# Performance work log

Hardware: AMD Instinct MI355X
Metric: run time of the kernel (lower is better)

Reference implementation:

```python
import jax, jax.numpy as jnp
import numpy as np

IN_DIM = 128
OUT_DIM = 128
B, N = 8, 2048
NEG_SLOPE = 0.2


def setup_inputs() -> dict:
    key = jax.random.key(0)
    k_h, k_adj, k_W, k_a = jax.random.split(key, 4)
    h = jax.random.normal(k_h, (B, N, IN_DIM), dtype=jnp.float32)
    adj = jax.random.randint(k_adj, (B, N, N), 0, 2, dtype=jnp.int32)
    # nn.Linear(in, out, bias=False): weight [out, in]
    W = jax.random.normal(k_W, (OUT_DIM, IN_DIM), dtype=jnp.float32) * (1.0 / np.sqrt(IN_DIM))
    # nn.Linear(2*out, 1, bias=False): weight [1, 2*out] -> store as vector [2*out]
    a = jax.random.normal(k_a, (2 * OUT_DIM,), dtype=jnp.float32) * (1.0 / np.sqrt(2 * OUT_DIM))
    return {"h": h, "adj": adj, "W": W, "a": a}


def reference(h, adj, W, a):
    # Wh: [B, N, Fo]
    Wh = jnp.einsum("bnf,of->bno", h, W)
    Fo = Wh.shape[-1]
    a_src, a_dst = a[:Fo], a[Fo:]
    # attn(cat([Wh_i, Wh_j])) == (Wh_i . a_src) + (Wh_j . a_dst) -- avoids [B,N,N,2F]
    s = Wh @ a_src  # [B, N]
    t = Wh @ a_dst  # [B, N]
    e = jax.nn.leaky_relu(s[:, :, None] + t[:, None, :], negative_slope=NEG_SLOPE)  # [B,N,N]
    e = jnp.where(adj == 0, -jnp.inf, e)
    alpha = jax.nn.softmax(e, axis=-1)
    alpha = jnp.nan_to_num(alpha, nan=0.0)  # rows with no neighbors -> 0
    return jnp.einsum("bnm,bmo->bno", alpha, Wh)
```

## Files before the change

kernel.cpp:

```cpp
#include <hip/hip_runtime.h>
#include <hip/hip_bf16.h>
#include <hip/hip_fp16.h>
#include <math.h>

#define B_ 8
#define N_ 2048
#define F_ 128

typedef __attribute__((ext_vector_type(8))) _Float16 half8;
typedef __attribute__((ext_vector_type(4))) float f32x4;

__global__ __launch_bounds__(256) void k_wh(
    const float* __restrict__ h, const float* __restrict__ W,
    const float* __restrict__ a,
    _Float16* __restrict__ WhH, float* __restrict__ sv, float* __restrict__ tv)
{
    __shared__ float h_s[64][129];
    __shared__ float Wt[128][68];
    __shared__ float wsm[128], wtm[128];
    __shared__ float sred[64][4], tred[64][4];

    const int t = threadIdx.x;
    const int rowblk = blockIdx.x >> 1;
    const int ohalf  = blockIdx.x & 1;
    const int r0 = rowblk * 64;

    {
        const int f = (t & 31) * 4;
        #pragma unroll
        for (int it = 0; it < 8; ++it) {
            const int r = (t >> 5) + it * 8;
            float4 v = *(const float4*)&h[(size_t)(r0 + r) * F_ + f];
            h_s[r][f] = v.x; h_s[r][f + 1] = v.y;
            h_s[r][f + 2] = v.z; h_s[r][f + 3] = v.w;
        }
    }
    {
        const int f = (t & 31) * 4;
        #pragma unroll
        for (int it = 0; it < 8; ++it) {
            const int o = (t >> 5) + it * 8;
            float4 v = *(const float4*)&W[(size_t)(ohalf * 64 + o) * F_ + f];
            Wt[f][o] = v.x; Wt[f + 1][o] = v.y;
            Wt[f + 2][o] = v.z; Wt[f + 3][o] = v.w;
        }
    }
    {
        const int f = t & 127;
        const int which = t >> 7;
        const float* av = a + which * 128;
        float acc = 0.f;
        for (int o = 0; o < 128; ++o)
            acc += W[(size_t)o * F_ + f] * av[o];
        if (which == 0) wsm[f] = acc; else wtm[f] = acc;
    }
    __syncthreads();

    const int o4 = t & 15;
    const int r4 = t >> 4;
    float acc[4][4];
    #pragma unroll
    for (int i = 0; i < 4; ++i)
        #pragma unroll
        for (int j = 0; j < 4; ++j) acc[i][j] = 0.f;

    #pragma unroll 4
    for (int k = 0; k < 128; ++k) {
        float4 w = *(const float4*)&Wt[k][o4 * 4];
        float h0 = h_s[r4 * 4 + 0][k];
        float h1 = h_s[r4 * 4 + 1][k];
        float h2 = h_s[r4 * 4 + 2][k];
        float h3 = h_s[r4 * 4 + 3][k];
        acc[0][0] += h0 * w.x; acc[0][1] += h0 * w.y; acc[0][2] += h0 * w.z; acc[0][3] += h0 * w.w;
        acc[1][0] += h1 * w.x; acc[1][1] += h1 * w.y; acc[1][2] += h1 * w.z; acc[1][3] += h1 * w.w;
        acc[2][0] += h2 * w.x; acc[2][1] += h2 * w.y; acc[2][2] += h2 * w.z; acc[2][3] += h2 * w.w;
        acc[3][0] += h3 * w.x; acc[3][1] += h3 * w.y; acc[3][2] += h3 * w.z; acc[3][3] += h3 * w.w;
    }

    {
        const int Rbase = r0 + r4 * 4;
        const int b    = Rbase >> 11;
        const int jj   = Rbase & 2047;
        const int jblk = jj >> 5;
        const int k8   = (jj >> 3) & 3;
        const int kk   = jj & 7;
        #pragma unroll
        for (int jo = 0; jo < 4; ++jo) {
            const int o = ohalf * 64 + o4 * 4 + jo;
            size_t off = ((size_t)(b * 64 + jblk) * 128 + o) * 32 + k8 * 8 + kk;
            union { _Float16 x[4]; uint2 u; } pk;
            pk.x[0] = (_Float16)acc[0][jo];
            pk.x[1] = (_Float16)acc[1][jo];
            pk.x[2] = (_Float16)acc[2][jo];
            pk.x[3] = (_Float16)acc[3][jo];
            *(uint2*)(WhH + off) = pk.u;
        }
    }

    {
        const int r = t & 63, part = t >> 6;
        float as_ = 0.f, at_ = 0.f;
        const int kb = part * 32;
        for (int k = kb; k < kb + 32; ++k) {
            float hv = h_s[r][k];
            as_ += hv * wsm[k];
            at_ += hv * wtm[k];
        }
        sred[r][part] = as_; tred[r][part] = at_;
    }
    __syncthreads();
    if (ohalf == 0 && t < 64) {
        sv[r0 + t] = sred[t][0] + sred[t][1] + sred[t][2] + sred[t][3];
        tv[r0 + t] = tred[t][0] + tred[t][1] + tred[t][2] + tred[t][3];
    }
}

__global__ __launch_bounds__(256, 4) void k_attn(
    const _Float16* __restrict__ WhH, const float* __restrict__ sv,
    const float* __restrict__ tv, const int* __restrict__ adj,
    float* __restrict__ out)
{
    __shared__ float redO[4][16][128];
    __shared__ float redL[4][16];
    __shared__ float tmr[4];

    const int t  = threadIdx.x;
    const int b  = blockIdx.x >> 7;
    const int i0 = (blockIdx.x & 127) * 16;
    const float* tb = tv + ((size_t)b << 11);

    float tm = -INFINITY;
    #pragma unroll
    for (int k = 0; k < 8; ++k) tm = fmaxf(tm, tb[t + k * 256]);
    #pragma unroll
    for (int k = 32; k; k >>= 1) tm = fmaxf(tm, __shfl_xor(tm, k, 64));
    if ((t & 63) == 0) tmr[t >> 6] = tm;
    __syncthreads();
    const float tmax = fmaxf(fmaxf(tmr[0], tmr[1]), fmaxf(tmr[2], tmr[3]));

    const int wv   = t >> 6;
    const int lane = t & 63;
    const int m_   = lane & 15;
    const int q_   = lane >> 4;

    const float s_i = sv[((size_t)b << 11) + i0 + m_];
    const float M_i = fmaxf(s_i + tmax, 0.f);

    const int jbase = wv * 512;
    const int* arow = adj + ((size_t)(((b << 11) + i0 + m_)) << 11) + q_ * 8;
    const float* tq = tb + q_ * 8;
    const _Float16* wbase = WhH + (((size_t)b * 64) << 12)
                          + (size_t)m_ * 32 + q_ * 8;

    f32x4 acc[8];
    #pragma unroll
    for (int n = 0; n < 8; ++n) acc[n] = (f32x4){0.f, 0.f, 0.f, 0.f};
    float lsum = 0.f;

    int4 aL = *(const int4*)&arow[jbase];
    int4 aH = *(const int4*)&arow[jbase + 4];

    for (int jj = 0; jj < 16; ++jj) {
        const int j0 = jbase + jj * 32;
        const int jn = jbase + ((jj + 1) & 15) * 32;
        int4 naL = *(const int4*)&arow[jn];
        int4 naH = *(const int4*)&arow[jn + 4];

        float4 tL = *(const float4*)&tq[j0];
        float4 tH = *(const float4*)&tq[j0 + 4];

        float e, p[8];
        e = s_i + tL.x; e = fmaxf(e, 0.2f * e); p[0] = aL.x ? __expf(e - M_i) : 0.f;
        e = s_i + tL.y; e = fmaxf(e, 0.2f * e); p[1] = aL.y ? __expf(e - M_i) : 0.f;
        e = s_i + tL.z; e = fmaxf(e, 0.2f * e); p[2] = aL.z ? __expf(e - M_i) : 0.f;
        e = s_i + tL.w; e = fmaxf(e, 0.2f * e); p[3] = aL.w ? __expf(e - M_i) : 0.f;
        e = s_i + tH.x; e = fmaxf(e, 0.2f * e); p[4] = aH.x ? __expf(e - M_i) : 0.f;
        e = s_i + tH.y; e = fmaxf(e, 0.2f * e); p[5] = aH.y ? __expf(e - M_i) : 0.f;
        e = s_i + tH.z; e = fmaxf(e, 0.2f * e); p[6] = aH.z ? __expf(e - M_i) : 0.f;
        e = s_i + tH.w; e = fmaxf(e, 0.2f * e); p[7] = aH.w ? __expf(e - M_i) : 0.f;

        lsum += ((p[0] + p[1]) + (p[2] + p[3])) + ((p[4] + p[5]) + (p[6] + p[7]));

        half8 af;
        #pragma unroll
        for (int k = 0; k < 8; ++k) af[k] = (_Float16)p[k];

        const _Float16* wb = wbase + ((size_t)(j0 >> 5) << 12);
        #pragma unroll
        for (int n = 0; n < 8; ++n) {
            half8 bf = *(const half8*)(wb + n * 512);
            acc[n] = __builtin_amdgcn_mfma_f32_16x16x32_f16(af, bf, acc[n], 0, 0, 0);
        }
        aL = naL; aH = naH;
    }

    lsum += __shfl_xor(lsum, 16, 64);
    lsum += __shfl_xor(lsum, 32, 64);
    if (q_ == 0) redL[wv][m_] = lsum;

    #pragma unroll
    for (int n = 0; n < 8; ++n)
        #pragma unroll
        for (int r = 0; r < 4; ++r)
            redO[wv][q_ * 4 + r][n * 16 + m_] = acc[n][r];
    __syncthreads();

    {
        const int row = t >> 4;
        const int c0  = (t & 15) * 8;
        const float li = redL[0][row] + redL[1][row] + redL[2][row] + redL[3][row];
        const float sc = li > 0.f ? 1.f / li : 0.f;
        float* op = out + (((size_t)((b << 11) + i0 + row)) << 7) + c0;
        #pragma unroll
        for (int c = 0; c < 8; ++c) {
            float v = redO[0][row][c0 + c] + redO[1][row][c0 + c]
                    + redO[2][row][c0 + c] + redO[3][row][c0 + c];
            op[c] = v * sc;
        }
    }
}

extern "C" void kernel_launch(void* const* d_in, const int* in_sizes, int n_in,
                              void* d_out, int out_size, void* d_ws, size_t ws_size,
                              hipStream_t stream) {
    const float* h   = (const float*)d_in[0];
    const int*   adj = (const int*)d_in[1];
    const float* W   = (const float*)d_in[2];
    const float* a   = (const float*)d_in[3];
    float* out = (float*)d_out;

    _Float16* WhH = (_Float16*)d_ws;
    float* sv = (float*)((char*)d_ws + (size_t)4 * 1024 * 1024);
    float* tv = sv + (size_t)B_ * N_;

    k_wh<<<512, 256, 0, stream>>>(h, W, a, WhH, sv, tv);
    k_attn<<<1024, 256, 0, stream>>>(WhH, sv, tv, adj, out);
}
```

Measured before the change: 242.4 us.

## Pack adjacency into bitmask in prep kernel and double rows per attention block

The first kernel gains extra blocks that ballot the int32 adjacency matrix into 64-bit bitmasks. The attention kernel then reads a 32x smaller mask instead of the full int adj rows. Each attention block now processes 32 query rows with two accumulator sets, so every loaded Wh tile is reused twice. The adj matrix is still read once in full, and the extra registers lower the occupancy bound to 2.

```diff
diff --git a/kernel.cpp b/kernel.cpp
--- a/kernel.cpp
+++ b/kernel.cpp
@@ -10,10 +10,11 @@
 typedef __attribute__((ext_vector_type(8))) _Float16 half8;
 typedef __attribute__((ext_vector_type(4))) float f32x4;
 
-__global__ __launch_bounds__(256) void k_wh(
+__global__ __launch_bounds__(256) void k_prep(
     const float* __restrict__ h, const float* __restrict__ W,
-    const float* __restrict__ a,
-    _Float16* __restrict__ WhH, float* __restrict__ sv, float* __restrict__ tv)
+    const float* __restrict__ a, const int* __restrict__ adj,
+    _Float16* __restrict__ WhH, float* __restrict__ sv, float* __restrict__ tv,
+    unsigned long long* __restrict__ mask)
 {
     __shared__ float h_s[64][129];
     __shared__ float Wt[128][68];
@@ -21,6 +22,26 @@
     __shared__ float sred[64][4], tred[64][4];
 
     const int t = threadIdx.x;
+
+    if (blockIdx.x >= 512) {
+        const int wv = t >> 6, lane = t & 63;
+        const int row = (blockIdx.x - 512) * 4 + wv;
+        const int* ap = adj + ((size_t)row << 11);
+        unsigned long long* mp = mask + (size_t)row * 32;
+        #pragma unroll
+        for (int it0 = 0; it0 < 32; it0 += 8) {
+            int v[8];
+            #pragma unroll
+            for (int u = 0; u < 8; ++u) v[u] = ap[(it0 + u) * 64 + lane];
+            #pragma unroll
+            for (int u = 0; u < 8; ++u) {
+                unsigned long long bm = __ballot(v[u] != 0);
+                if (lane == 0) mp[it0 + u] = bm;
+            }
+        }
+        return;
+    }
+
     const int rowblk = blockIdx.x >> 1;
     const int ohalf  = blockIdx.x & 1;
     const int r0 = rowblk * 64;
@@ -115,18 +136,18 @@
     }
 }
 
-__global__ __launch_bounds__(256, 4) void k_attn(
+__global__ __launch_bounds__(256, 2) void k_attn(
     const _Float16* __restrict__ WhH, const float* __restrict__ sv,
-    const float* __restrict__ tv, const int* __restrict__ adj,
+    const float* __restrict__ tv, const unsigned int* __restrict__ maskd,
     float* __restrict__ out)
 {
-    __shared__ float redO[4][16][128];
-    __shared__ float redL[4][16];
+    __shared__ float redO[4][32][128];
+    __shared__ float redL[4][32];
     __shared__ float tmr[4];
 
     const int t  = threadIdx.x;
-    const int b  = blockIdx.x >> 7;
-    const int i0 = (blockIdx.x & 127) * 16;
+    const int b  = blockIdx.x >> 6;
+    const int i0 = (blockIdx.x & 63) * 32;
     const float* tb = tv + ((size_t)b << 11);
 
     float tm = -INFINITY;
@@ -143,76 +164,85 @@
     const int m_   = lane & 15;
     const int q_   = lane >> 4;
 
-    const float s_i = sv[((size_t)b << 11) + i0 + m_];
-    const float M_i = fmaxf(s_i + tmax, 0.f);
-
-    const int jbase = wv * 512;
-    const int* arow = adj + ((size_t)(((b << 11) + i0 + m_)) << 11) + q_ * 8;
-    const float* tq = tb + q_ * 8;
-    const _Float16* wbase = WhH + (((size_t)b * 64) << 12)
+    const float s0 = sv[((size_t)b << 11) + i0 + m_];
+    const float s1 = sv[((size_t)b << 11) + i0 + 16 + m_];
+    const float M0 = fmaxf(s0 + tmax, 0.f);
+    const float M1 = fmaxf(s1 + tmax, 0.f);
+
+    const unsigned int* mrow0 =
+        maskd + (size_t)(((b << 11) + i0 + m_)) * 64 + wv * 16;
+    const unsigned int* mrow1 = mrow0 + 16 * 64;
+    const float* tq = tb + wv * 512 + q_ * 8;
+    const _Float16* wbase = WhH + (((size_t)b * 64 + wv * 16) << 12)
                           + (size_t)m_ * 32 + q_ * 8;
 
-    f32x4 acc[8];
-    #pragma unroll
-    for (int n = 0; n < 8; ++n) acc[n] = (f32x4){0.f, 0.f, 0.f, 0.f};
-    float lsum = 0.f;
-
-    int4 aL = *(const int4*)&arow[jbase];
-    int4 aH = *(const int4*)&arow[jbase + 4];
+    f32x4 acc0[8], acc1[8];
+    #pragma unroll
+    for (int n = 0; n < 8; ++n) {
+        acc0[n] = (f32x4){0.f, 0.f, 0.f, 0.f};
+        acc1[n] = (f32x4){0.f, 0.f, 0.f, 0.f};
+    }
+    float lsum0 = 0.f, lsum1 = 0.f;
+
+    unsigned int mc0 = mrow0[0], mc1 = mrow1[0];
 
     for (int jj = 0; jj < 16; ++jj) {
-        const int j0 = jbase + jj * 32;
-        const int jn = jbase + ((jj + 1) & 15) * 32;
-        int4 naL = *(const int4*)&arow[jn];
-        int4 naH = *(const int4*)&arow[jn + 4];
-
-        float4 tL = *(const float4*)&tq[j0];
-        float4 tH = *(const float4*)&tq[j0 + 4];
-
-        float e, p[8];
-        e = s_i + tL.x; e = fmaxf(e, 0.2f * e); p[0] = aL.x ? __expf(e - M_i) : 0.f;
-        e = s_i + tL.y; e = fmaxf(e, 0.2f * e); p[1] = aL.y ? __expf(e - M_i) : 0.f;
-        e = s_i + tL.z; e = fmaxf(e, 0.2f * e); p[2] = aL.z ? __expf(e - M_i) : 0.f;
-        e = s_i + tL.w; e = fmaxf(e, 0.2f * e); p[3] = aL.w ? __expf(e - M_i) : 0.f;
-        e = s_i + tH.x; e = fmaxf(e, 0.2f * e); p[4] = aH.x ? __expf(e - M_i) : 0.f;
-        e = s_i + tH.y; e = fmaxf(e, 0.2f * e); p[5] = aH.y ? __expf(e - M_i) : 0.f;
-        e = s_i + tH.z; e = fmaxf(e, 0.2f * e); p[6] = aH.z ? __expf(e - M_i) : 0.f;
-        e = s_i + tH.w; e = fmaxf(e, 0.2f * e); p[7] = aH.w ? __expf(e - M_i) : 0.f;
-
-        lsum += ((p[0] + p[1]) + (p[2] + p[3])) + ((p[4] + p[5]) + (p[6] + p[7]));
-
-        half8 af;
-        #pragma unroll
-        for (int k = 0; k < 8; ++k) af[k] = (_Float16)p[k];
-
-        const _Float16* wb = wbase + ((size_t)(j0 >> 5) << 12);
+        const int nxt = (jj + 1) & 15;
+        unsigned int mn0 = mrow0[nxt];
+        unsigned int mn1 = mrow1[nxt];
+
+        const _Float16* wb = wbase + ((size_t)jj << 12);
+        half8 bf[8];
+        #pragma unroll
+        for (int n = 0; n < 8; ++n)
+            bf[n] = *(const half8*)(wb + n * 512);
+
+        float4 tL = *(const float4*)&tq[jj * 32];
+        float4 tH = *(const float4*)&tq[jj * 32 + 4];
+        const unsigned int bq0 = mc0 >> (q_ * 8);
+        const unsigned int bq1 = mc1 >> (q_ * 8);
+
+        float tvk[8] = {tL.x, tL.y, tL.z, tL.w, tH.x, tH.y, tH.z, tH.w};
+        half8 af0, af1;
+        #pragma unroll
+        for (int k = 0; k < 8; ++k) {
+            float e0 = s0 + tvk[k]; e0 = fmaxf(e0, 0.2f * e0);
+            float p0 = (bq0 >> k) & 1 ? __expf(e0 - M0) : 0.f;
+            float e1 = s1 + tvk[k]; e1 = fmaxf(e1, 0.2f * e1);
+            float p1 = (bq1 >> k) & 1 ? __expf(e1 - M1) : 0.f;
+            lsum0 += p0; lsum1 += p1;
+            af0[k] = (_Float16)p0; af1[k] = (_Float16)p1;
+        }
+
         #pragma unroll
         for (int n = 0; n < 8; ++n) {
-            half8 bf = *(const half8*)(wb + n * 512);
-            acc[n] = __builtin_amdgcn_mfma_f32_16x16x32_f16(af, bf, acc[n], 0, 0, 0);
-        }
-        aL = naL; aH = naH;
-    }
-
-    lsum += __shfl_xor(lsum, 16, 64);
-    lsum += __shfl_xor(lsum, 32, 64);
-    if (q_ == 0) redL[wv][m_] = lsum;
+            acc0[n] = __builtin_amdgcn_mfma_f32_16x16x32_f16(af0, bf[n], acc0[n], 0, 0, 0);
+            acc1[n] = __builtin_amdgcn_mfma_f32_16x16x32_f16(af1, bf[n], acc1[n], 0, 0, 0);
+        }
+        mc0 = mn0; mc1 = mn1;
+    }
+
+    lsum0 += __shfl_xor(lsum0, 16, 64); lsum0 += __shfl_xor(lsum0, 32, 64);
+    lsum1 += __shfl_xor(lsum1, 16, 64); lsum1 += __shfl_xor(lsum1, 32, 64);
+    if (q_ == 0) { redL[wv][m_] = lsum0; redL[wv][16 + m_] = lsum1; }
 
     #pragma unroll
     for (int n = 0; n < 8; ++n)
         #pragma unroll
-        for (int r = 0; r < 4; ++r)
-            redO[wv][q_ * 4 + r][n * 16 + m_] = acc[n][r];
-    __syncthreads();
-
-    {
-        const int row = t >> 4;
-        const int c0  = (t & 15) * 8;
+        for (int r = 0; r < 4; ++r) {
+            redO[wv][q_ * 4 + r][n * 16 + m_]      = acc0[n][r];
+            redO[wv][16 + q_ * 4 + r][n * 16 + m_] = acc1[n][r];
+        }
+    __syncthreads();
+
+    {
+        const int row = t >> 3;
+        const int c0  = (t & 7) * 16;
         const float li = redL[0][row] + redL[1][row] + redL[2][row] + redL[3][row];
         const float sc = li > 0.f ? 1.f / li : 0.f;
         float* op = out + (((size_t)((b << 11) + i0 + row)) << 7) + c0;
         #pragma unroll
-        for (int c = 0; c < 8; ++c) {
+        for (int c = 0; c < 16; ++c) {
             float v = redO[0][row][c0 + c] + redO[1][row][c0 + c]
                     + redO[2][row][c0 + c] + redO[3][row][c0 + c];
             op[c] = v * sc;
@@ -232,7 +262,9 @@
     _Float16* WhH = (_Float16*)d_ws;
     float* sv = (float*)((char*)d_ws + (size_t)4 * 1024 * 1024);
     float* tv = sv + (size_t)B_ * N_;
-
-    k_wh<<<512, 256, 0, stream>>>(h, W, a, WhH, sv, tv);
-    k_attn<<<1024, 256, 0, stream>>>(WhH, sv, tv, adj, out);
+    unsigned long long* mask =
+        (unsigned long long*)((char*)d_ws + (size_t)4 * 1024 * 1024 + 256 * 1024);
+
+    k_prep<<<4608, 256, 0, stream>>>(h, W, a, adj, WhH, sv, tv, mask);
+    k_attn<<<512, 256, 0, stream>>>(WhH, sv, tv, (const unsigned int*)mask, out);
 }
```

After: 248.6 us. 2.6% more time.

## Split attention over key chunks with LDS-staged Wh and separate combine kernel

Applied to the files above, without the earlier changes.

The attention kernel now assigns each block 64 query rows and one quarter of the key range, stages the fp16 Wh tiles in double-buffered shared memory so the four waves share them, and caches the t vector in LDS. Per-chunk unnormalized outputs and row sums go to workspace, and a new combine kernel adds the four partials and normalizes. The aim is to cut redundant global loads of Wh across waves. The cost is two barriers per iteration, a 32 MB partial buffer with its extra write and read traffic, and a third launch.

```diff
diff --git a/kernel.cpp b/kernel.cpp
--- a/kernel.cpp
+++ b/kernel.cpp
@@ -10,7 +10,7 @@
 typedef __attribute__((ext_vector_type(8))) _Float16 half8;
 typedef __attribute__((ext_vector_type(4))) float f32x4;
 
-__global__ __launch_bounds__(256) void k_wh(
+__global__ __launch_bounds__(256) void k_gemm(
     const float* __restrict__ h, const float* __restrict__ W,
     const float* __restrict__ a,
     _Float16* __restrict__ WhH, float* __restrict__ sv, float* __restrict__ tv)
@@ -115,18 +115,22 @@
     }
 }
 
-__global__ __launch_bounds__(256, 4) void k_attn(
+__global__ __launch_bounds__(256, 3) void k_attn(
     const _Float16* __restrict__ WhH, const float* __restrict__ sv,
     const float* __restrict__ tv, const int* __restrict__ adj,
-    float* __restrict__ out)
+    float* __restrict__ Po, float* __restrict__ Pl)
 {
-    __shared__ float redO[4][16][128];
-    __shared__ float redL[4][16];
+    __shared__ _Float16 whS[2][4096];
+    __shared__ float tS[512];
     __shared__ float tmr[4];
 
-    const int t  = threadIdx.x;
-    const int b  = blockIdx.x >> 7;
-    const int i0 = (blockIdx.x & 127) * 16;
+    const int t   = threadIdx.x;
+    const int b   = blockIdx.x & 7;
+    const int rem = blockIdx.x >> 3;
+    const int i0  = (rem & 31) * 64;
+    const int jh  = rem >> 5;
+    const int jbase = jh * 512;
+
     const float* tb = tv + ((size_t)b << 11);
 
     float tm = -INFINITY;
@@ -135,89 +139,107 @@
     #pragma unroll
     for (int k = 32; k; k >>= 1) tm = fmaxf(tm, __shfl_xor(tm, k, 64));
     if ((t & 63) == 0) tmr[t >> 6] = tm;
-    __syncthreads();
-    const float tmax = fmaxf(fmaxf(tmr[0], tmr[1]), fmaxf(tmr[2], tmr[3]));
+
+    tS[t]       = tb[jbase + t];
+    tS[t + 256] = tb[jbase + t + 256];
 
     const int wv   = t >> 6;
     const int lane = t & 63;
     const int m_   = lane & 15;
     const int q_   = lane >> 4;
 
-    const float s_i = sv[((size_t)b << 11) + i0 + m_];
-    const float M_i = fmaxf(s_i + tmax, 0.f);
-
-    const int jbase = wv * 512;
-    const int* arow = adj + ((size_t)(((b << 11) + i0 + m_)) << 11) + q_ * 8;
-    const float* tq = tb + q_ * 8;
-    const _Float16* wbase = WhH + (((size_t)b * 64) << 12)
-                          + (size_t)m_ * 32 + q_ * 8;
+    const int   girow = (b << 11) + i0 + wv * 16 + m_;
+    const float s_i   = sv[girow];
+    const int*  arow  = adj + ((size_t)girow << 11) + jbase + q_ * 8;
+
+    const _Float16* whc = WhH + (((size_t)b * 64 + jh * 16) << 12);
+
+    {
+        uint4 w0 = *(const uint4*)(whc + (size_t)t * 8);
+        uint4 w1 = *(const uint4*)(whc + (size_t)(t + 256) * 8);
+        *(uint4*)&whS[0][t * 8]         = w0;
+        *(uint4*)&whS[0][(t + 256) * 8] = w1;
+    }
+    int4 aC0 = *(const int4*)(arow);
+    int4 aC1 = *(const int4*)(arow + 4);
+    __syncthreads();
+    const float M_i = fmaxf(s_i + fmaxf(fmaxf(tmr[0], tmr[1]), fmaxf(tmr[2], tmr[3])), 0.f);
 
     f32x4 acc[8];
     #pragma unroll
     for (int n = 0; n < 8; ++n) acc[n] = (f32x4){0.f, 0.f, 0.f, 0.f};
     float lsum = 0.f;
 
-    int4 aL = *(const int4*)&arow[jbase];
-    int4 aH = *(const int4*)&arow[jbase + 4];
-
     for (int jj = 0; jj < 16; ++jj) {
-        const int j0 = jbase + jj * 32;
-        const int jn = jbase + ((jj + 1) & 15) * 32;
-        int4 naL = *(const int4*)&arow[jn];
-        int4 naH = *(const int4*)&arow[jn + 4];
-
-        float4 tL = *(const float4*)&tq[j0];
-        float4 tH = *(const float4*)&tq[j0 + 4];
-
-        float e, p[8];
-        e = s_i + tL.x; e = fmaxf(e, 0.2f * e); p[0] = aL.x ? __expf(e - M_i) : 0.f;
-        e = s_i + tL.y; e = fmaxf(e, 0.2f * e); p[1] = aL.y ? __expf(e - M_i) : 0.f;
-        e = s_i + tL.z; e = fmaxf(e, 0.2f * e); p[2] = aL.z ? __expf(e - M_i) : 0.f;
-        e = s_i + tL.w; e = fmaxf(e, 0.2f * e); p[3] = aL.w ? __expf(e - M_i) : 0.f;
-        e = s_i + tH.x; e = fmaxf(e, 0.2f * e); p[4] = aH.x ? __expf(e - M_i) : 0.f;
-        e = s_i + tH.y; e = fmaxf(e, 0.2f * e); p[5] = aH.y ? __expf(e - M_i) : 0.f;
-        e = s_i + tH.z; e = fmaxf(e, 0.2f * e); p[6] = aH.z ? __expf(e - M_i) : 0.f;
-        e = s_i + tH.w; e = fmaxf(e, 0.2f * e); p[7] = aH.w ? __expf(e - M_i) : 0.f;
-
-        lsum += ((p[0] + p[1]) + (p[2] + p[3])) + ((p[4] + p[5]) + (p[6] + p[7]));
-
+        const int cur  = jj & 1;
+        const int nxt  = (jj + 1) & 15;
+        const int nbuf = (jj + 1) & 1;
+
+        const _Float16* whn = whc + ((size_t)nxt << 12);
+        uint4 w0 = *(const uint4*)(whn + (size_t)t * 8);
+        uint4 w1 = *(const uint4*)(whn + (size_t)(t + 256) * 8);
+        int4 aN0 = *(const int4*)(arow + nxt * 32);
+        int4 aN1 = *(const int4*)(arow + nxt * 32 + 4);
+
+        float4 tL = *(const float4*)&tS[jj * 32 + q_ * 8];
+        float4 tH = *(const float4*)&tS[jj * 32 + q_ * 8 + 4];
+        float tvk[8] = {tL.x, tL.y, tL.z, tL.w, tH.x, tH.y, tH.z, tH.w};
+        int   avk[8] = {aC0.x, aC0.y, aC0.z, aC0.w, aC1.x, aC1.y, aC1.z, aC1.w};
         half8 af;
         #pragma unroll
-        for (int k = 0; k < 8; ++k) af[k] = (_Float16)p[k];
-
-        const _Float16* wb = wbase + ((size_t)(j0 >> 5) << 12);
+        for (int k = 0; k < 8; ++k) {
+            float e = s_i + tvk[k]; e = fmaxf(e, 0.2f * e);
+            float p = avk[k] ? __expf(e - M_i) : 0.f;
+            lsum += p;
+            af[k] = (_Float16)p;
+        }
+
         #pragma unroll
         for (int n = 0; n < 8; ++n) {
-            half8 bf = *(const half8*)(wb + n * 512);
+            half8 bf = *(const half8*)&whS[cur][n * 512 + m_ * 32 + q_ * 8];
             acc[n] = __builtin_amdgcn_mfma_f32_16x16x32_f16(af, bf, acc[n], 0, 0, 0);
         }
-        aL = naL; aH = naH;
+
+        __syncthreads();
+        *(uint4*)&whS[nbuf][t * 8]         = w0;
+        *(uint4*)&whS[nbuf][(t + 256) * 8] = w1;
+        aC0 = aN0; aC1 = aN1;
+        __syncthreads();
     }
 
     lsum += __shfl_xor(lsum, 16, 64);
     lsum += __shfl_xor(lsum, 32, 64);
-    if (q_ == 0) redL[wv][m_] = lsum;
-
+    if (q_ == 0) Pl[(size_t)jh * (B_ * N_) + girow] = lsum;
+
+    float* po = Po + (size_t)jh * ((size_t)B_ * N_ * F_)
+              + (((size_t)((b << 11) + i0 + wv * 16)) << 7);
     #pragma unroll
     for (int n = 0; n < 8; ++n)
         #pragma unroll
         for (int r = 0; r < 4; ++r)
-            redO[wv][q_ * 4 + r][n * 16 + m_] = acc[n][r];
-    __syncthreads();
-
-    {
-        const int row = t >> 4;
-        const int c0  = (t & 15) * 8;
-        const float li = redL[0][row] + redL[1][row] + redL[2][row] + redL[3][row];
-        const float sc = li > 0.f ? 1.f / li : 0.f;
-        float* op = out + (((size_t)((b << 11) + i0 + row)) << 7) + c0;
-        #pragma unroll
-        for (int c = 0; c < 8; ++c) {
-            float v = redO[0][row][c0 + c] + redO[1][row][c0 + c]
-                    + redO[2][row][c0 + c] + redO[3][row][c0 + c];
-            op[c] = v * sc;
-        }
-    }
+            po[(size_t)(q_ * 4 + r) * F_ + n * 16 + m_] = acc[n][r];
+}
+
+__global__ __launch_bounds__(256) void k_comb(
+    const float* __restrict__ Po, const float* __restrict__ Pl,
+    float* __restrict__ out)
+{
+    const int idx = blockIdx.x * 256 + threadIdx.x;
+    const int gi  = idx >> 5;
+    const int o4  = (idx & 31) * 4;
+    const size_t stride = (size_t)B_ * N_ * F_;
+
+    float4 v = *(const float4*)&Po[(size_t)gi * F_ + o4];
+    float  l = Pl[gi];
+    #pragma unroll
+    for (int jh = 1; jh < 4; ++jh) {
+        float4 u = *(const float4*)&Po[jh * stride + (size_t)gi * F_ + o4];
+        v.x += u.x; v.y += u.y; v.z += u.z; v.w += u.w;
+        l += Pl[jh * (B_ * N_) + gi];
+    }
+    const float sc = l > 0.f ? 1.f / l : 0.f;
+    float4 r = {v.x * sc, v.y * sc, v.z * sc, v.w * sc};
+    *(float4*)&out[(size_t)gi * F_ + o4] = r;
 }
 
 extern "C" void kernel_launch(void* const* d_in, const int* in_sizes, int n_in,
@@ -229,10 +251,14 @@
     const float* a   = (const float*)d_in[3];
     float* out = (float*)d_out;
 
-    _Float16* WhH = (_Float16*)d_ws;
-    float* sv = (float*)((char*)d_ws + (size_t)4 * 1024 * 1024);
+    char* ws = (char*)d_ws;
+    _Float16* WhH = (_Float16*)ws;
+    float* sv = (float*)(ws + (size_t)4 * 1024 * 1024);
     float* tv = sv + (size_t)B_ * N_;
-
-    k_wh<<<512, 256, 0, stream>>>(h, W, a, WhH, sv, tv);
-    k_attn<<<1024, 256, 0, stream>>>(WhH, sv, tv, adj, out);
-}
+    float* Po = (float*)(ws + (size_t)8 * 1024 * 1024);
+    float* Pl = (float*)(ws + (size_t)40 * 1024 * 1024);
+
+    k_gemm<<<512, 256, 0, stream>>>(h, W, a, WhH, sv, tv);
+    k_attn<<<1024, 256, 0, stream>>>(WhH, sv, tv, adj, Po, Pl);
+    k_comb<<<2048, 256, 0, stream>>>(Po, Pl, out);
+}
```

Result: faster. 235.1 us (-3.0%).

## Software-pipeline adj and Wh loads in attention kernel, cache t in LDS

Applied to the files above, without the earlier changes.

The attention kernel now prefetches adjacency rows four chunks ahead and Wh B-fragments two chunks ahead into register ring buffers, fully unrolling the j-loop. It stages the t vector in shared memory instead of re-reading it from global memory, and interleaves batch across block indices. Occupancy hint drops from 4 to 3 blocks per CU to make room for the extra registers. The goal is to hide memory latency on the dominant adj stream, at the cost of higher register pressure and lower occupancy.

```diff
diff --git a/kernel.cpp b/kernel.cpp
--- a/kernel.cpp
+++ b/kernel.cpp
@@ -10,7 +10,7 @@
 typedef __attribute__((ext_vector_type(8))) _Float16 half8;
 typedef __attribute__((ext_vector_type(4))) float f32x4;
 
-__global__ __launch_bounds__(256) void k_wh(
+__global__ __launch_bounds__(256) void k_gemm(
     const float* __restrict__ h, const float* __restrict__ W,
     const float* __restrict__ a,
     _Float16* __restrict__ WhH, float* __restrict__ sv, float* __restrict__ tv)
@@ -115,23 +115,28 @@
     }
 }
 
-__global__ __launch_bounds__(256, 4) void k_attn(
+__global__ __launch_bounds__(256, 3) void k_attn(
     const _Float16* __restrict__ WhH, const float* __restrict__ sv,
     const float* __restrict__ tv, const int* __restrict__ adj,
     float* __restrict__ out)
 {
     __shared__ float redO[4][16][128];
     __shared__ float redL[4][16];
+    __shared__ float tS[2048];
     __shared__ float tmr[4];
 
     const int t  = threadIdx.x;
-    const int b  = blockIdx.x >> 7;
-    const int i0 = (blockIdx.x & 127) * 16;
+    const int b  = blockIdx.x & 7;
+    const int i0 = (blockIdx.x >> 3) * 16;
     const float* tb = tv + ((size_t)b << 11);
 
     float tm = -INFINITY;
     #pragma unroll
-    for (int k = 0; k < 8; ++k) tm = fmaxf(tm, tb[t + k * 256]);
+    for (int k = 0; k < 8; ++k) {
+        float v = tb[t + k * 256];
+        tS[t + k * 256] = v;
+        tm = fmaxf(tm, v);
+    }
     #pragma unroll
     for (int k = 32; k; k >>= 1) tm = fmaxf(tm, __shfl_xor(tm, k, 64));
     if ((t & 63) == 0) tmr[t >> 6] = tm;
@@ -142,56 +147,68 @@
     const int lane = t & 63;
     const int m_   = lane & 15;
     const int q_   = lane >> 4;
-
-    const float s_i = sv[((size_t)b << 11) + i0 + m_];
-    const float M_i = fmaxf(s_i + tmax, 0.f);
-
     const int jbase = wv * 512;
-    const int* arow = adj + ((size_t)(((b << 11) + i0 + m_)) << 11) + q_ * 8;
-    const float* tq = tb + q_ * 8;
-    const _Float16* wbase = WhH + (((size_t)b * 64) << 12)
-                          + (size_t)m_ * 32 + q_ * 8;
+
+    const int   girow = (b << 11) + i0 + m_;
+    const float s_i   = sv[girow];
+    const float M_i   = fmaxf(s_i + tmax, 0.f);
+
+    const int*      arow = adj + ((size_t)girow << 11) + jbase + q_ * 8;
+    const _Float16* whc  = WhH + (((size_t)b * 64 + wv * 16) << 12)
+                         + (size_t)m_ * 32 + q_ * 8;
 
     f32x4 acc[8];
     #pragma unroll
     for (int n = 0; n < 8; ++n) acc[n] = (f32x4){0.f, 0.f, 0.f, 0.f};
     float lsum = 0.f;
 
-    int4 aL = *(const int4*)&arow[jbase];
-    int4 aH = *(const int4*)&arow[jbase + 4];
-
+    int4  pa0[4], pa1[4];
+    half8 pb[2][8];
+
+    #pragma unroll
+    for (int c = 0; c < 4; ++c) {
+        pa0[c] = *(const int4*)(arow + c * 32);
+        pa1[c] = *(const int4*)(arow + c * 32 + 4);
+    }
+    #pragma unroll
+    for (int c = 0; c < 2; ++c)
+        #pragma unroll
+        for (int n = 0; n < 8; ++n)
+            pb[c][n] = *(const half8*)(whc + ((size_t)c << 12) + n * 512);
+
+    #pragma unroll
     for (int jj = 0; jj < 16; ++jj) {
-        const int j0 = jbase + jj * 32;
-        const int jn = jbase + ((jj + 1) & 15) * 32;
-        int4 naL = *(const int4*)&arow[jn];
-        int4 naH = *(const int4*)&arow[jn + 4];
-
-        float4 tL = *(const float4*)&tq[j0];
-        float4 tH = *(const float4*)&tq[j0 + 4];
-
-        float e, p[8];
-        e = s_i + tL.x; e = fmaxf(e, 0.2f * e); p[0] = aL.x ? __expf(e - M_i) : 0.f;
-        e = s_i + tL.y; e = fmaxf(e, 0.2f * e); p[1] = aL.y ? __expf(e - M_i) : 0.f;
-        e = s_i + tL.z; e = fmaxf(e, 0.2f * e); p[2] = aL.z ? __expf(e - M_i) : 0.f;
-        e = s_i + tL.w; e = fmaxf(e, 0.2f * e); p[3] = aL.w ? __expf(e - M_i) : 0.f;
-        e = s_i + tH.x; e = fmaxf(e, 0.2f * e); p[4] = aH.x ? __expf(e - M_i) : 0.f;
-        e = s_i + tH.y; e = fmaxf(e, 0.2f * e); p[5] = aH.y ? __expf(e - M_i) : 0.f;
-        e = s_i + tH.z; e = fmaxf(e, 0.2f * e); p[6] = aH.z ? __expf(e - M_i) : 0.f;
-        e = s_i + tH.w; e = fmaxf(e, 0.2f * e); p[7] = aH.w ? __expf(e - M_i) : 0.f;
-
-        lsum += ((p[0] + p[1]) + (p[2] + p[3])) + ((p[4] + p[5]) + (p[6] + p[7]));
-
+        const int sA = jj & 3;
+        const int sB = jj & 1;
+        const int nA = (jj + 4) & 15;
+        const int nB = (jj + 2) & 15;
+
+        int4 a0 = pa0[sA], a1 = pa1[sA];
+        half8 bf[8];
+        #pragma unroll
+        for (int n = 0; n < 8; ++n) bf[n] = pb[sB][n];
+
+        pa0[sA] = *(const int4*)(arow + nA * 32);
+        pa1[sA] = *(const int4*)(arow + nA * 32 + 4);
+        #pragma unroll
+        for (int n = 0; n < 8; ++n)
+            pb[sB][n] = *(const half8*)(whc + ((size_t)nB << 12) + n * 512);
+
+        const float* tp = &tS[jbase + jj * 32 + q_ * 8];
+        float tvk[8] = {tp[0], tp[1], tp[2], tp[3], tp[4], tp[5], tp[6], tp[7]};
+        int   avk[8] = {a0.x, a0.y, a0.z, a0.w, a1.x, a1.y, a1.z, a1.w};
         half8 af;
         #pragma unroll
-        for (int k = 0; k < 8; ++k) af[k] = (_Float16)p[k];
-
-        const _Float16* wb = wbase + ((size_t)(j0 >> 5) << 12);
-        #pragma unroll
-        for (int n = 0; n < 8; ++n) {
-            half8 bf = *(const half8*)(wb + n * 512);
-            acc[n] = __builtin_amdgcn_mfma_f32_16x16x32_f16(af, bf, acc[n], 0, 0, 0);
-        }
-        aL = naL; aH = naH;
+        for (int k = 0; k < 8; ++k) {
+            float e = s_i + tvk[k]; e = fmaxf(e, 0.2f * e);
+            float p = avk[k] ? __expf(e - M_i) : 0.f;
+            lsum += p;
+            af[k] = (_Float16)p;
+        }
+
+        #pragma unroll
+        for (int n = 0; n < 8; ++n)
+            acc[n] = __builtin_amdgcn_mfma_f32_16x16x32_f16(af, bf[n], acc[n], 0, 0, 0);
     }
 
     lsum += __shfl_xor(lsum, 16, 64);
@@ -229,10 +246,11 @@
     const float* a   = (const float*)d_in[3];
     float* out = (float*)d_out;
 
-    _Float16* WhH = (_Float16*)d_ws;
-    float* sv = (float*)((char*)d_ws + (size_t)4 * 1024 * 1024);
+    char* ws = (char*)d_ws;
+    _Float16* WhH = (_Float16*)ws;
+    float* sv = (float*)(ws + (size_t)4 * 1024 * 1024);
     float* tv = sv + (size_t)B_ * N_;
 
-    k_wh<<<512, 256, 0, stream>>>(h, W, a, WhH, sv, tv);
+    k_gemm<<<512, 256, 0, stream>>>(h, W, a, WhH, sv, tv);
     k_attn<<<1024, 256, 0, stream>>>(WhH, sv, tv, adj, out);
 }
```

New measurement: 243.6 us. No clear change (+0.5%).
